# Optimization experiments

Hardware: AMD Instinct MI355X
Metric: run time of the kernel (lower is better)

Reference implementation:

```python
import jax, jax.numpy as jnp
import numpy as np

B, C, L = 16, 128, 512
F = L // 2 + 1  # 257

def setup_inputs() -> dict:
    key = jax.random.key(0)
    k1, k2, k3 = jax.random.split(key, 3)
    x = jax.random.normal(k1, (B, C, L), dtype=jnp.float32)
    A = jax.random.normal(k2, (F, F), dtype=jnp.float32)
    gumbel_u = jax.random.uniform(k3, (B, C, C, 2), dtype=jnp.float32)
    return {"x": x, "A": A, "gumbel_u": gumbel_u}

def reference(x, A, gumbel_u):
    # --- calculate_prob_distance ---
    xf = jnp.abs(jnp.fft.rfft(x, axis=-1))                 # (b, c, f)
    diff = xf[:, None, :, :] - xf[:, :, None, :]           # (b, c, c, f): x1 - x2
    temp = jnp.einsum('bijf,gf->bijg', diff, A)            # diff @ A.T
    dist = jnp.sum(temp * temp, axis=-1)                   # (b, c, c)
    exp_dist = 1.0 / (dist + 3e-8)
    c = exp_dist.shape[-1]
    eye = jnp.eye(c, dtype=exp_dist.dtype)
    exp_dist = exp_dist * (1.0 - eye)
    exp_max = jax.lax.stop_gradient(jnp.max(exp_dist, axis=-1, keepdims=True))
    p = exp_dist / (exp_max + 1e-8)
    p = (p + eye) * 0.99
    # --- bernoulli_gumbel_rsample (hard gumbel-softmax, tau=1) ---
    logits = jnp.log(p + 1e-8) - jnp.log(1.0 - p + 1e-8)
    logits_pair = jnp.stack([logits, -logits], axis=-1)    # (b, c, c, 2)
    g = -jnp.log(-jnp.log(gumbel_u + 1e-20) + 1e-20)       # gumbel noise
    y = jax.nn.softmax(logits_pair + g, axis=-1)
    y_hard = jax.nn.one_hot(jnp.argmax(y, axis=-1), 2, dtype=y.dtype)
    samples = y_hard + y - jax.lax.stop_gradient(y)        # straight-through
    binary_mask = samples[..., 0]                          # (b, c, c)
    mask = binary_mask[:, None, :, :]                      # (b, 1, c, c)
    return mask
```

## Files before the change

### kernel.cpp

```cpp
#include <hip/hip_runtime.h>

#define LN   512
#define FB   257
#define CB   128
#define NROW 2048
#define KF   260
#define NP   272

typedef double double4_t __attribute__((ext_vector_type(4)));

__global__ __launch_bounds__(128)
void k_fftprep(const float* __restrict__ x, const float* __restrict__ A,
               double* __restrict__ xft, double* __restrict__ At_d) {
    const int bx  = blockIdx.x;
    const int tid = threadIdx.x;

    if (bx >= 1024) {
        if (bx < 1577) {
            int idx = (bx - 1024) * 128 + tid;
            if (idx < KF * NP) {
                int f = idx / NP, g = idx - f * NP;
                At_d[idx] = (f < FB && g < FB) ? (double)A[g * FB + f] : 0.0;
            }
        } else {
            int idx = (bx - 1577) * 128 + tid;
            xft[(size_t)FB * NROW + idx] = 0.0;
        }
        return;
    }

    __shared__ double2 a[LN];
    __shared__ double2 tw[256];
    const int r0 = bx * 2;

    const double PI = 3.14159265358979323846264338327950288;
    for (int t = tid; t < 256; t += 128) {
        double s, c;
        sincos(-2.0 * PI * (double)t / 512.0, &s, &c);
        tw[t] = make_double2(c, s);
    }

    const float* x0 = x + (size_t)r0 * LN;
    const float* x1 = x0 + LN;
    #pragma unroll
    for (int q = 0; q < 4; ++q) {
        int n = tid + 128 * q;
        int r = (int)(__brev((unsigned)n) >> 23);
        a[r] = make_double2((double)x0[n], (double)x1[n]);
    }
    __syncthreads();

    #pragma unroll
    for (int s = 1; s <= 7; s += 2) {
        const int h    = 1 << (s - 1);
        const int k    = tid & (h - 1);
        const int grp  = tid >> (s - 1);
        const int base = (grp << (s + 1)) + k;

        double2 a0 = a[base];
        double2 a1 = a[base + h];
        double2 a2 = a[base + 2 * h];
        double2 a3 = a[base + 3 * h];
        double2 w1  = tw[k << (9 - s)];
        double2 w20 = tw[k << (8 - s)];
        double2 w21 = tw[(k + h) << (8 - s)];

        double vr = a1.x * w1.x - a1.y * w1.y;
        double vi = a1.x * w1.y + a1.y * w1.x;
        double2 t0 = make_double2(a0.x + vr, a0.y + vi);
        double2 t1 = make_double2(a0.x - vr, a0.y - vi);
        vr = a3.x * w1.x - a3.y * w1.y;
        vi = a3.x * w1.y + a3.y * w1.x;
        double2 t2 = make_double2(a2.x + vr, a2.y + vi);
        double2 t3 = make_double2(a2.x - vr, a2.y - vi);

        vr = t2.x * w20.x - t2.y * w20.y;
        vi = t2.x * w20.y + t2.y * w20.x;
        a[base]         = make_double2(t0.x + vr, t0.y + vi);
        a[base + 2 * h] = make_double2(t0.x - vr, t0.y - vi);
        vr = t3.x * w21.x - t3.y * w21.y;
        vi = t3.x * w21.y + t3.y * w21.x;
        a[base + h]     = make_double2(t1.x + vr, t1.y + vi);
        a[base + 3 * h] = make_double2(t1.x - vr, t1.y - vi);
        __syncthreads();
    }

    #pragma unroll
    for (int u = 0; u < 2; ++u) {
        int t = tid + 128 * u;
        double2 w  = tw[t];
        double2 uu = a[t];
        double2 v  = a[t + 256];
        double vr = v.x * w.x - v.y * w.y;
        double vi = v.x * w.y + v.y * w.x;
        a[t]       = make_double2(uu.x + vr, uu.y + vi);
        a[t + 256] = make_double2(uu.x - vr, uu.y - vi);
    }
    __syncthreads();

    for (int k = tid; k < FB; k += 128) {
        int m = (LN - k) & (LN - 1);
        double2 zk = a[k];
        double2 zm = a[m];
        double xr = 0.5 * (zk.x + zm.x);
        double xi = 0.5 * (zk.y - zm.y);
        double yr = 0.5 * (zk.y + zm.y);
        double yi = 0.5 * (zm.x - zk.x);
        double m0 = sqrt(xr * xr + xi * xi);
        double m1 = sqrt(yr * yr + yi * yi);
        *(double2*)&xft[(size_t)k * NROW + r0] = make_double2(m0, m1);
    }
}

__global__ __launch_bounds__(256)
void k_zmat(const double* __restrict__ xft, const double* __restrict__ At_d,
            double* __restrict__ Zt) {
    const int bx  = blockIdx.x;
    const int tid = threadIdx.x;
    const int w   = tid >> 6;
    const int l   = tid & 63;
    const int q   = l >> 4;
    const int m   = l & 15;

    const int gt  = bx % 17;
    const int cht = (bx / 17) * 4 + w;
    const int g0  = gt * 16;
    const int ch0 = cht * 16;

    const double* pa = At_d + (size_t)q * NP + g0 + m;
    const double* pb = xft + (size_t)q * NROW + ch0 + m;

    double4_t acc = {0.0, 0.0, 0.0, 0.0};
    double a0 = pa[0],              b0 = pb[0];
    double a1 = pa[(size_t)4 * NP], b1 = pb[(size_t)4 * NROW];
    for (int it = 0; it < 63; ++it) {
        double a2 = pa[(size_t)(it + 2) * 4 * NP];
        double b2 = pb[(size_t)(it + 2) * 4 * NROW];
        acc = __builtin_amdgcn_mfma_f64_16x16x4f64(a0, b0, acc, 0, 0, 0);
        a0 = a1; a1 = a2; b0 = b1; b1 = b2;
    }
    acc = __builtin_amdgcn_mfma_f64_16x16x4f64(a0, b0, acc, 0, 0, 0);
    acc = __builtin_amdgcn_mfma_f64_16x16x4f64(a1, b1, acc, 0, 0, 0);

    const int b   = cht >> 3;
    const int chL = ((cht & 7) << 4) + m;
    double* zp = Zt + ((size_t)b * NP + g0 + q) * CB + chL;
    #pragma unroll
    for (int r = 0; r < 4; ++r) zp[(size_t)(4 * r) * CB] = acc[r];
}

__global__ __launch_bounds__(256)
void k_gram(const double* __restrict__ Zt, double* __restrict__ G) {
    const int bx  = blockIdx.x;
    const int tid = threadIdx.x;
    const int w   = tid >> 6;
    const int l   = tid & 63;
    const int q   = l >> 4;
    const int m   = l & 15;

    const int b  = bx >> 4;
    const int it = (bx >> 1) & 7;
    const int jt = (bx & 1) * 4 + w;
    const int i0 = it * 16, j0 = jt * 16;

    const double* zb = Zt + (size_t)b * NP * CB;
    const double* pa = zb + (size_t)q * CB + i0 + m;
    const double* pb = zb + (size_t)q * CB + j0 + m;

    double4_t acc = {0.0, 0.0, 0.0, 0.0};
    double a0 = pa[0],    b0 = pb[0];
    double a1 = pa[512],  b1 = pb[512];
    double a2 = pa[1024], b2 = pb[1024];
    double a3 = pa[1536], b3 = pb[1536];
    for (int t2 = 0; t2 < 61; ++t2) {
        double an = pa[(size_t)(t2 + 4) * 512];
        double bn = pb[(size_t)(t2 + 4) * 512];
        acc = __builtin_amdgcn_mfma_f64_16x16x4f64(a0, b0, acc, 0, 0, 0);
        a0 = a1; a1 = a2; a2 = a3; a3 = an;
        b0 = b1; b1 = b2; b2 = b3; b3 = bn;
    }
    acc = __builtin_amdgcn_mfma_f64_16x16x4f64(a0, b0, acc, 0, 0, 0);
    acc = __builtin_amdgcn_mfma_f64_16x16x4f64(a1, b1, acc, 0, 0, 0);
    acc = __builtin_amdgcn_mfma_f64_16x16x4f64(a2, b2, acc, 0, 0, 0);
    acc = __builtin_amdgcn_mfma_f64_16x16x4f64(a3, b3, acc, 0, 0, 0);

    double* gp = G + ((size_t)(b * CB + i0 + q)) * CB + j0 + m;
    #pragma unroll
    for (int r = 0; r < 4; ++r) gp[(size_t)(4 * r) * CB] = acc[r];
}

__global__ __launch_bounds__(128)
void k_mask2(const double* __restrict__ G,
             const float* __restrict__ gu, float* __restrict__ out) {
    __shared__ double sn[CB];
    __shared__ double wmax[2];
    const int bi = blockIdx.x;
    const int i  = bi & (CB - 1);
    const int b  = bi >> 7;
    const int j  = threadIdx.x;

    double nj = G[((size_t)(b * CB + j)) * CB + j];
    double Gv = G[(size_t)bi * CB + j];
    sn[j] = nj;
    __syncthreads();
    double ni = sn[i];
    double dist = ni + nj - 2.0 * Gv;

    double ed = 1.0 / (dist + 3e-8);
    if (j == i) ed = 0.0;

    double m = ed;
    #pragma unroll
    for (int off = 32; off >= 1; off >>= 1)
        m = fmax(m, __shfl_xor(m, off, 64));
    if ((j & 63) == 0) wmax[j >> 6] = m;
    __syncthreads();
    double emax = fmax(wmax[0], wmax[1]);

    double p = ed / (emax + 1e-8);
    if (j == i) p += 1.0;
    p *= 0.99;
    double L = log((p + 1e-8) / (1.0 - p + 1e-8));

    float2 u2 = ((const float2*)gu)[(size_t)bi * CB + j];
    double w0 = -log((double)u2.x + 1e-20);
    double w1 = -log((double)u2.y + 1e-20);
    double R = log((w0 + 1e-20) / (w1 + 1e-20));

    out[(size_t)bi * CB + j] = (2.0 * L >= R) ? 1.0f : 0.0f;
}

extern "C" void kernel_launch(void* const* d_in, const int* in_sizes, int n_in,
                              void* d_out, int out_size, void* d_ws, size_t ws_size,
                              hipStream_t stream) {
    const float* x  = (const float*)d_in[0];
    const float* A  = (const float*)d_in[1];
    const float* gu = (const float*)d_in[2];
    float* out = (float*)d_out;

    char* base = (char*)d_ws;
    const size_t szAt  = (size_t)KF * NP * 8;
    const size_t szXft = (size_t)KF * NROW * 8;
    const size_t szZt  = (size_t)16 * NP * CB * 8;

    double* At_d = (double*)base;
    double* xft  = (double*)(base + szAt);
    double* Zt   = (double*)(base + szAt + szXft);
    double* G    = (double*)(base + szAt + szXft + szZt);

    hipLaunchKernelGGL(k_fftprep, dim3(1625), dim3(128), 0, stream, x, A, xft, At_d);
    hipLaunchKernelGGL(k_zmat,    dim3(544),  dim3(256), 0, stream, xft, At_d, Zt);
    hipLaunchKernelGGL(k_gram,    dim3(256),  dim3(256), 0, stream, Zt, G);
    hipLaunchKernelGGL(k_mask2,   dim3(2048), dim3(128), 0, stream, G, gu, out);
}
```

Measured before the change: 53.12 us.

## Fuse zmat, gram and mask kernels into one cooperative kernel with grid sync

```diff
diff --git a/kernel.cpp b/kernel.cpp
--- a/kernel.cpp
+++ b/kernel.cpp
@@ -1,4 +1,5 @@
 #include <hip/hip_runtime.h>
+#include <hip/hip_cooperative_groups.h>
 
 #define LN   512
 #define FB   257
@@ -112,9 +113,16 @@
     }
 }
 
-__global__ __launch_bounds__(256)
-void k_zmat(const double* __restrict__ xft, const double* __restrict__ At_d,
-            double* __restrict__ Zt) {
+__global__ __launch_bounds__(512)
+void k_zgm(const double* __restrict__ xft, const double* __restrict__ At_d,
+           double* __restrict__ Zt, double* __restrict__ G,
+           const float* __restrict__ gu, float* __restrict__ out) {
+    namespace cg = cooperative_groups;
+    cg::grid_group grid = cg::this_grid();
+
+    __shared__ double sn[4][CB];
+    __shared__ double wm[4][2];
+
     const int bx  = blockIdx.x;
     const int tid = threadIdx.x;
     const int w   = tid >> 6;
@@ -122,112 +130,115 @@
     const int q   = l >> 4;
     const int m   = l & 15;
 
-    const int gt  = bx % 17;
-    const int cht = (bx / 17) * 4 + w;
-    const int g0  = gt * 16;
-    const int ch0 = cht * 16;
-
-    const double* pa = At_d + (size_t)q * NP + g0 + m;
-    const double* pb = xft + (size_t)q * NROW + ch0 + m;
-
-    double4_t acc = {0.0, 0.0, 0.0, 0.0};
-    double a0 = pa[0],              b0 = pb[0];
-    double a1 = pa[(size_t)4 * NP], b1 = pb[(size_t)4 * NROW];
-    for (int it = 0; it < 63; ++it) {
-        double a2 = pa[(size_t)(it + 2) * 4 * NP];
-        double b2 = pb[(size_t)(it + 2) * 4 * NROW];
-        acc = __builtin_amdgcn_mfma_f64_16x16x4f64(a0, b0, acc, 0, 0, 0);
-        a0 = a1; a1 = a2; b0 = b1; b1 = b2;
-    }
-    acc = __builtin_amdgcn_mfma_f64_16x16x4f64(a0, b0, acc, 0, 0, 0);
-    acc = __builtin_amdgcn_mfma_f64_16x16x4f64(a1, b1, acc, 0, 0, 0);
-
-    const int b   = cht >> 3;
-    const int chL = ((cht & 7) << 4) + m;
-    double* zp = Zt + ((size_t)b * NP + g0 + q) * CB + chL;
-    #pragma unroll
-    for (int r = 0; r < 4; ++r) zp[(size_t)(4 * r) * CB] = acc[r];
-}
-
-__global__ __launch_bounds__(256)
-void k_gram(const double* __restrict__ Zt, double* __restrict__ G) {
-    const int bx  = blockIdx.x;
-    const int tid = threadIdx.x;
-    const int w   = tid >> 6;
-    const int l   = tid & 63;
-    const int q   = l >> 4;
-    const int m   = l & 15;
-
-    const int b  = bx >> 4;
-    const int it = (bx >> 1) & 7;
-    const int jt = (bx & 1) * 4 + w;
-    const int i0 = it * 16, j0 = jt * 16;
-
-    const double* zb = Zt + (size_t)b * NP * CB;
-    const double* pa = zb + (size_t)q * CB + i0 + m;
-    const double* pb = zb + (size_t)q * CB + j0 + m;
-
-    double4_t acc = {0.0, 0.0, 0.0, 0.0};
-    double a0 = pa[0],    b0 = pb[0];
-    double a1 = pa[512],  b1 = pb[512];
-    double a2 = pa[1024], b2 = pb[1024];
-    double a3 = pa[1536], b3 = pb[1536];
-    for (int t2 = 0; t2 < 61; ++t2) {
-        double an = pa[(size_t)(t2 + 4) * 512];
-        double bn = pb[(size_t)(t2 + 4) * 512];
-        acc = __builtin_amdgcn_mfma_f64_16x16x4f64(a0, b0, acc, 0, 0, 0);
-        a0 = a1; a1 = a2; a2 = a3; a3 = an;
-        b0 = b1; b1 = b2; b2 = b3; b3 = bn;
-    }
-    acc = __builtin_amdgcn_mfma_f64_16x16x4f64(a0, b0, acc, 0, 0, 0);
-    acc = __builtin_amdgcn_mfma_f64_16x16x4f64(a1, b1, acc, 0, 0, 0);
-    acc = __builtin_amdgcn_mfma_f64_16x16x4f64(a2, b2, acc, 0, 0, 0);
-    acc = __builtin_amdgcn_mfma_f64_16x16x4f64(a3, b3, acc, 0, 0, 0);
-
-    double* gp = G + ((size_t)(b * CB + i0 + q)) * CB + j0 + m;
-    #pragma unroll
-    for (int r = 0; r < 4; ++r) gp[(size_t)(4 * r) * CB] = acc[r];
-}
-
-__global__ __launch_bounds__(128)
-void k_mask2(const double* __restrict__ G,
-             const float* __restrict__ gu, float* __restrict__ out) {
-    __shared__ double sn[CB];
-    __shared__ double wmax[2];
-    const int bi = blockIdx.x;
-    const int i  = bi & (CB - 1);
-    const int b  = bi >> 7;
-    const int j  = threadIdx.x;
-
-    double nj = G[((size_t)(b * CB + j)) * CB + j];
-    double Gv = G[(size_t)bi * CB + j];
-    sn[j] = nj;
-    __syncthreads();
-    double ni = sn[i];
-    double dist = ni + nj - 2.0 * Gv;
-
-    double ed = 1.0 / (dist + 3e-8);
-    if (j == i) ed = 0.0;
-
-    double m = ed;
-    #pragma unroll
-    for (int off = 32; off >= 1; off >>= 1)
-        m = fmax(m, __shfl_xor(m, off, 64));
-    if ((j & 63) == 0) wmax[j >> 6] = m;
-    __syncthreads();
-    double emax = fmax(wmax[0], wmax[1]);
-
-    double p = ed / (emax + 1e-8);
-    if (j == i) p += 1.0;
-    p *= 0.99;
-    double L = log((p + 1e-8) / (1.0 - p + 1e-8));
-
-    float2 u2 = ((const float2*)gu)[(size_t)bi * CB + j];
-    double w0 = -log((double)u2.x + 1e-20);
-    double w1 = -log((double)u2.y + 1e-20);
-    double R = log((w0 + 1e-20) / (w1 + 1e-20));
-
-    out[(size_t)bi * CB + j] = (2.0 * L >= R) ? 1.0f : 0.0f;
+    {
+        const int W = bx * 8 + w;
+        for (int T = W; T < 2176; T += 2048) {
+            const int gt  = T % 17;
+            const int cht = T / 17;
+            const int g0  = gt * 16;
+            const int ch0 = cht * 16;
+
+            const double* pa = At_d + (size_t)q * NP + g0 + m;
+            const double* pb = xft + (size_t)q * NROW + ch0 + m;
+
+            double4_t acc = {0.0, 0.0, 0.0, 0.0};
+            double a0 = pa[0],              b0 = pb[0];
+            double a1 = pa[(size_t)4 * NP], b1 = pb[(size_t)4 * NROW];
+            for (int it = 0; it < 63; ++it) {
+                double a2 = pa[(size_t)(it + 2) * 4 * NP];
+                double b2 = pb[(size_t)(it + 2) * 4 * NROW];
+                acc = __builtin_amdgcn_mfma_f64_16x16x4f64(a0, b0, acc, 0, 0, 0);
+                a0 = a1; a1 = a2; b0 = b1; b1 = b2;
+            }
+            acc = __builtin_amdgcn_mfma_f64_16x16x4f64(a0, b0, acc, 0, 0, 0);
+            acc = __builtin_amdgcn_mfma_f64_16x16x4f64(a1, b1, acc, 0, 0, 0);
+
+            const int b   = cht >> 3;
+            const int chL = ((cht & 7) << 4) + m;
+            double* zp = Zt + ((size_t)b * NP + g0 + q) * CB + chL;
+            #pragma unroll
+            for (int r = 0; r < 4; ++r) zp[(size_t)(4 * r) * CB] = acc[r];
+        }
+    }
+    grid.sync();
+
+    {
+        const int W = bx * 8 + w;
+        if (W < 1024) {
+            const int b  = W >> 6;
+            const int it = (W >> 3) & 7;
+            const int jt = W & 7;
+            const int i0 = it * 16, j0 = jt * 16;
+
+            const double* zb = Zt + (size_t)b * NP * CB;
+            const double* pa = zb + (size_t)q * CB + i0 + m;
+            const double* pb = zb + (size_t)q * CB + j0 + m;
+
+            double4_t acc = {0.0, 0.0, 0.0, 0.0};
+            double a0 = pa[0],    b0 = pb[0];
+            double a1 = pa[512],  b1 = pb[512];
+            double a2 = pa[1024], b2 = pb[1024];
+            double a3 = pa[1536], b3 = pb[1536];
+            for (int t2 = 0; t2 < 61; ++t2) {
+                double an = pa[(size_t)(t2 + 4) * 512];
+                double bn = pb[(size_t)(t2 + 4) * 512];
+                acc = __builtin_amdgcn_mfma_f64_16x16x4f64(a0, b0, acc, 0, 0, 0);
+                a0 = a1; a1 = a2; a2 = a3; a3 = an;
+                b0 = b1; b1 = b2; b2 = b3; b3 = bn;
+            }
+            acc = __builtin_amdgcn_mfma_f64_16x16x4f64(a0, b0, acc, 0, 0, 0);
+            acc = __builtin_amdgcn_mfma_f64_16x16x4f64(a1, b1, acc, 0, 0, 0);
+            acc = __builtin_amdgcn_mfma_f64_16x16x4f64(a2, b2, acc, 0, 0, 0);
+            acc = __builtin_amdgcn_mfma_f64_16x16x4f64(a3, b3, acc, 0, 0, 0);
+
+            double* gp = G + ((size_t)(b * CB + i0 + q)) * CB + j0 + m;
+            #pragma unroll
+            for (int r = 0; r < 4; ++r) gp[(size_t)(4 * r) * CB] = acc[r];
+        }
+    }
+    grid.sync();
+
+    {
+        const int slot = tid >> 7;
+        const int j    = tid & 127;
+        #pragma unroll
+        for (int rep = 0; rep < 2; ++rep) {
+            const int bi = bx * 8 + rep * 4 + slot;
+            const int i  = bi & (CB - 1);
+            const int b  = bi >> 7;
+
+            double nj = G[((size_t)(b * CB + j)) * CB + j];
+            double Gv = G[(size_t)bi * CB + j];
+            sn[slot][j] = nj;
+            __syncthreads();
+            double ni = sn[slot][i];
+            double dist = ni + nj - 2.0 * Gv;
+
+            double ed = 1.0 / (dist + 3e-8);
+            if (j == i) ed = 0.0;
+
+            double mx = ed;
+            #pragma unroll
+            for (int off = 32; off >= 1; off >>= 1)
+                mx = fmax(mx, __shfl_xor(mx, off, 64));
+            if ((j & 63) == 0) wm[slot][j >> 6] = mx;
+            __syncthreads();
+            double emax = fmax(wm[slot][0], wm[slot][1]);
+
+            double p = ed / (emax + 1e-8);
+            if (j == i) p += 1.0;
+            p *= 0.99;
+            double L = log((p + 1e-8) / (1.0 - p + 1e-8));
+
+            float2 u2 = ((const float2*)gu)[(size_t)bi * CB + j];
+            double w0 = -log((double)u2.x + 1e-20);
+            double w1 = -log((double)u2.y + 1e-20);
+            double R = log((w0 + 1e-20) / (w1 + 1e-20));
+
+            out[(size_t)bi * CB + j] = (2.0 * L >= R) ? 1.0f : 0.0f;
+            __syncthreads();
+        }
+    }
 }
 
 extern "C" void kernel_launch(void* const* d_in, const int* in_sizes, int n_in,
@@ -249,7 +260,9 @@
     double* G    = (double*)(base + szAt + szXft + szZt);
 
     hipLaunchKernelGGL(k_fftprep, dim3(1625), dim3(128), 0, stream, x, A, xft, At_d);
-    hipLaunchKernelGGL(k_zmat,    dim3(544),  dim3(256), 0, stream, xft, At_d, Zt);
-    hipLaunchKernelGGL(k_gram,    dim3(256),  dim3(256), 0, stream, Zt, G);
-    hipLaunchKernelGGL(k_mask2,   dim3(2048), dim3(128), 0, stream, G, gu, out);
+
+    void* args[] = {(void*)&xft, (void*)&At_d, (void*)&Zt, (void*)&G,
+                    (void*)&gu, (void*)&out};
+    hipLaunchCooperativeKernel((const void*)k_zgm, dim3(256), dim3(512),
+                               args, 0, stream);
 }
```

Result: slower. 131.8 us (+148.1%).
